# Kernel tuning notes

Hardware: AMD Instinct MI355X
Metric: run time of the kernel (lower is better)

Reference implementation:

```python
import jax, jax.numpy as jnp
import numpy as np

COL = 14
NJ = 14
SIGMA = 1.0
RADIUS = 4  # int(truncate*sigma + 0.5) with scipy defaults truncate=4.0
B = 8192
C = NJ + 4  # 14 joint channels + 4 group channels


def _gauss_kernel():
    x = np.arange(-RADIUS, RADIUS + 1).astype(np.float32)
    k = np.exp(-0.5 * x * x / (SIGMA * SIGMA))
    return jnp.asarray(k / k.sum(), jnp.float32)


def _gaussian_filter(x):
    # x: [N, H, W]; scipy gaussian_filter(sigma=1.0, mode='reflect') == symmetric pad + separable conv
    k = _gauss_kernel()
    xp = jnp.pad(x, ((0, 0), (RADIUS, RADIUS), (RADIUS, RADIUS)), mode='symmetric')
    y = jax.lax.conv_general_dilated(xp[:, None, :, :], k.reshape(1, 1, 2 * RADIUS + 1, 1), (1, 1), 'VALID')
    y = jax.lax.conv_general_dilated(y, k.reshape(1, 1, 1, 2 * RADIUS + 1), (1, 1), 'VALID')
    return y[:, 0]


def setup_inputs() -> dict:
    key = jax.random.key(0)
    k1, k2, k3, k4 = jax.random.split(key, 4)
    return {
        'os': jax.random.normal(k1, (B, 2 * NJ, COL, COL), dtype=jnp.float32),
        'h': jax.random.normal(k2, (B, C, COL, COL), dtype=jnp.float32),
        't': jax.random.uniform(k3, (B, NJ, 2), dtype=jnp.float32),
        'v': jax.random.randint(k4, (B, NJ, 2), 0, 2, dtype=jnp.int32),
    }


def reference(os, h, t, v):
    b = h.shape[0]
    # pixel indices: int() truncation then clamp to [0, 13]
    ti = jax.lax.stop_gradient(t) * COL
    idx = jnp.clip(ti.astype(jnp.int32), 0, COL - 1)
    xi, yi = idx[..., 0], idx[..., 1]
    vis = (v[..., 0] == 1)  # [B, NJ]

    ar = jnp.arange(COL)
    onehot = ((ar[:, None] == yi[..., None, None]) & (ar[None, :] == xi[..., None, None])).astype(h.dtype)  # [B,NJ,14,14]
    joint_hot = onehot * vis[..., None, None].astype(h.dtype)

    # 4 group channels from joints 0:3, 3:6, 6:9, 9:12 (set to 1, i.e. max, not add)
    ghot = joint_hot[:, :12].reshape(b, 4, 3, COL, COL).max(axis=2)
    gvis = vis[:, :12].reshape(b, 4, 3).any(axis=2)

    hot = jnp.concatenate([joint_hot, ghot], axis=1)        # [B, 18, 14, 14]
    mask = jnp.concatenate([vis, gvis], axis=1)             # [B, 18]

    filt = _gaussian_filter(hot.reshape(b * C, COL, COL)).reshape(b, C, COL, COL)
    mn = filt.min(axis=(-2, -1), keepdims=True)
    mx = filt.max(axis=(-2, -1), keepdims=True)
    denom = jnp.where(mx - mn == 0, jnp.ones_like(mx), mx - mn)
    tt = jnp.where(mask[..., None, None], (filt - mn) / denom, jnp.zeros_like(filt))

    diff = (h - tt) * mask[..., None, None].astype(h.dtype)
    n1 = v.sum().astype(h.dtype) / 2
    return jnp.sum(diff * diff) / n1
```

## Files before the change

### kernel.cpp

```cpp
#include <hip/hip_runtime.h>

#define NB   8192
#define NJ   14
#define NC   18
#define PIX  196
#define CHE  (NC * PIX)
#define CHB  (PIX * 4)
#define BPB  8
#define NBLK (NB / BPB)
#define GSTR 16
#define ZROW 14

#define WSUM_INV 0.398943491f

__global__ __launch_bounds__(512, 8) void mse_partial_kernel(
    const float* __restrict__ h, const float* __restrict__ t,
    const int* __restrict__ v, float2* __restrict__ partials)
{
    __shared__ float  gs[15 * GSTR];
    __shared__ float  gmx[14];
    __shared__ int    scode[BPB * 16];
    __shared__ float2 list[BPB * NC];
    __shared__ float  wvs[BPB];
    __shared__ float  wred[BPB];

    const int tid = threadIdx.x;
    const int b0  = blockIdx.x * BPB;
    const int w   = tid >> 6, lane = tid & 63;
    const int b   = b0 + w;

    if (tid < 15 * GSTR) {
        int p = tid >> 4, r = tid & 15;
        int rc = (r < 14) ? r : (r - 14);
        float val = 0.f;
        if (p < 14) {
            const float wl[9] = {0.00033546262f, 0.011108997f, 0.13533528f, 0.60653066f,
                                 1.0f, 0.60653066f, 0.13533528f, 0.011108997f, 0.00033546262f};
            float acc = 0.f;
            #pragma unroll
            for (int k = 0; k < 9; k++) {
                int m  = rc + k - 4;
                int sm = m < 0 ? (-m - 1) : (m > 13 ? 27 - m : m);
                if (sm == p) acc += wl[k];
            }
            val = acc * WSUM_INV;
        }
        gs[tid] = val;
    }
    __syncthreads();
    if (tid < 14) {
        float mx = 0.f;
        #pragma unroll
        for (int r = 0; r < 14; r++) mx = fmaxf(mx, gs[tid * GSTR + r]);
        gmx[tid] = mx;
    }
    __syncthreads();

    int rb_[4], cb_[4];
    #pragma unroll
    for (int q = 0; q < 4; q++) {
        int e = lane + 64 * q;
        int ee = (e < PIX) ? e : PIX - 1;
        int rr = ee / 14, cc = ee - 14 * rr;
        rb_[q] = rr << 2; cb_[q] = cc << 2;
    }

    int xi = 0, yi = 0, vis = 0, vy = 0;
    if (lane < NJ) {
        float2 tv = ((const float2*)t)[b * NJ + lane];
        int2   vv = ((const int2*)v)[b * NJ + lane];
        xi = (int)(tv.x * 14.0f); xi = xi < 0 ? 0 : (xi > 13 ? 13 : xi);
        yi = (int)(tv.y * 14.0f); yi = yi < 0 ? 0 : (yi > 13 ? 13 : yi);
        vis = (vv.x == 1); vy = (vv.y == 1);
    }
    if (lane < NJ) scode[w * 16 + lane] = (vis << 8) | (xi << 4) | yi;
    {
        unsigned long long bx = __ballot(lane < NJ && vis);
        unsigned long long by = __ballot(lane < NJ && vy);
        if (lane == 0) wvs[w] = (float)(__popcll(bx) + __popcll(by));
    }

    float inv_c = 0.f;
    int   pos_c = 0, act_c = 0, np_c = 0;
    if (lane < NJ && vis) {
        inv_c = 1.f / (gmx[yi] * gmx[xi]);
        act_c = 1; np_c = 1;
        pos_c = yi | (xi << 4) | (ZROW << 8) | (ZROW << 16);
    }
    for (int gi = 0; gi < 4; gi++) {
        int c0  = __builtin_amdgcn_readfirstlane(scode[w * 16 + 3 * gi]);
        int c1_ = __builtin_amdgcn_readfirstlane(scode[w * 16 + 3 * gi + 1]);
        int c2  = __builtin_amdgcn_readfirstlane(scode[w * 16 + 3 * gi + 2]);
        int packed = 0, np = 0;
        if (c0 & 0x100) { packed = c0 & 0xFF; np = 1; }
        if (c1_ & 0x100) {
            int pc = c1_ & 0xFF;
            bool dup = (np > 0) && ((packed & 0xFF) == pc);
            if (!dup) { packed |= pc << (8 * np); np++; }
        }
        if (c2 & 0x100) {
            int pc = c2 & 0xFF;
            bool dup = false;
            for (int s = 0; s < np; s++) if (((packed >> (8 * s)) & 0xFF) == pc) dup = true;
            if (!dup) { packed |= pc << (8 * np); np++; }
        }
        int pp = packed;
        if (np < 2) pp |= ZROW << 8;
        if (np < 3) pp |= ZROW << 16;

        float mx = 1.f;
        if (np == 1) {
            int y = packed & 15, x = (packed >> 4) & 15;
            mx = gmx[y] * gmx[x];
        } else if (np >= 2) {
            const int o0 = ( pp        & 15) << 6, p0 = ((pp >> 4)  & 15) << 6;
            const int o1 = ((pp >> 8)  & 15) << 6, p1 = ((pp >> 12) & 15) << 6;
            const int o2 = ((pp >> 16) & 15) << 6, p2 = ((pp >> 20) & 15) << 6;
            const char* g8 = (const char*)gs;
            float lmx = 0.f;
            #pragma unroll
            for (int q2 = 0; q2 < 4; q2++) {
                float f = *(const float*)(g8 + o0 + rb_[q2]) * *(const float*)(g8 + p0 + cb_[q2])
                        + *(const float*)(g8 + o1 + rb_[q2]) * *(const float*)(g8 + p1 + cb_[q2])
                        + *(const float*)(g8 + o2 + rb_[q2]) * *(const float*)(g8 + p2 + cb_[q2]);
                lmx = fmaxf(lmx, f);
            }
            #pragma unroll
            for (int m = 1; m < 64; m <<= 1)
                lmx = fmaxf(lmx, __shfl_xor(lmx, m));
            mx = lmx;
        }
        if (lane == NJ + gi && np > 0) {
            inv_c = 1.f / mx; act_c = 1; np_c = np;
            pos_c = pp;
        }
    }
    unsigned long long b1 = __ballot(act_c && np_c == 1);
    unsigned long long bX = __ballot(act_c && np_c >= 2);
    const int c1 = __popcll(b1);
    const int cT = c1 + __popcll(bX);
    unsigned long long below = (1ull << lane) - 1ull;
    if (act_c) {
        int idx = (np_c == 1) ? __popcll(b1 & below) : c1 + __popcll(bX & below);
        float2 e;
        e.x = inv_c;
        e.y = __int_as_float(pos_c | (lane << 24));
        list[w * NC + idx] = e;
    }

    const char* hb   = (const char*)(h + (size_t)b * CHE);
    const int  lane49 = lane < 48 ? lane : 48;
    const bool lv     = (lane < 49);
    const int  pix0   = lane49 * 4;
    const int  rr0    = pix0 / 14;
    const int  cc0    = pix0 - 14 * rr0;
    const bool wrap   = (cc0 == 12);
    const int  voff   = lane49 * 16;
    const int  brr = rr0 << 2, bcc = cc0 << 2;
    const int  lbase  = w * NC;
    const char* g8 = (const char*)gs;
    float acc = 0.f;

    const int nfull = c1 & ~3;
    for (int base = 0; base < nfull; base += 4) {
        float inv[4];
        int   syo[4], sxo[4], sb[4];
        float4 hv[4];
        #pragma unroll
        for (int u = 0; u < 4; u++) {
            float2 mv = list[lbase + base + u];
            inv[u] = mv.x;
            int sp = __builtin_amdgcn_readfirstlane(__float_as_int(mv.y));
            syo[u] = ( sp       & 15) << 6;
            sxo[u] = ((sp >> 4) & 15) << 6;
            sb[u]  = (sp >> 24) * CHB;
            hv[u] = *(const float4*)(hb + sb[u] + voff);
        }
        #pragma unroll
        for (int u = 0; u < 4; u++) {
            const float* ry = (const float*)(g8 + syo[u] + brr);
            const char*  rx = g8 + sxo[u] + bcc;
            float2 xA = *(const float2*)rx;
            float2 xB = *(const float2*)(rx + 8);
            float wy0 = ry[0], wy1 = ry[1];
            float wy0i = wy0 * inv[u];
            float wyCi = (wrap ? wy1 : wy0) * inv[u];
            float d0 = fmaf(-wy0i, xA.x, hv[u].x);
            float d1 = fmaf(-wy0i, xA.y, hv[u].y);
            float d2 = fmaf(-wyCi, xB.x, hv[u].z);
            float d3 = fmaf(-wyCi, xB.y, hv[u].w);
            acc += fmaf(d0, d0, fmaf(d1, d1, fmaf(d2, d2, d3 * d3)));
        }
    }
    if (c1 & 3) {
        float inv[4];
        int   syo[4], sxo[4], sb[4], ok[4];
        float4 hv[4];
        #pragma unroll
        for (int u = 0; u < 4; u++) {
            int ee = nfull + u;
            ok[u] = (ee < c1);
            float2 mv = list[lbase + (ok[u] ? ee : c1 - 1)];
            inv[u] = mv.x;
            int sp = __builtin_amdgcn_readfirstlane(__float_as_int(mv.y));
            syo[u] = ( sp       & 15) << 6;
            sxo[u] = ((sp >> 4) & 15) << 6;
            sb[u]  = (sp >> 24) * CHB;
            hv[u] = *(const float4*)(hb + sb[u] + voff);
        }
        #pragma unroll
        for (int u = 0; u < 4; u++) {
            const float* ry = (const float*)(g8 + syo[u] + brr);
            const char*  rx = g8 + sxo[u] + bcc;
            float2 xA = *(const float2*)rx;
            float2 xB = *(const float2*)(rx + 8);
            float wy0 = ry[0], wy1 = ry[1];
            float wy0i = wy0 * inv[u];
            float wyCi = (wrap ? wy1 : wy0) * inv[u];
            float d0 = fmaf(-wy0i, xA.x, hv[u].x);
            float d1 = fmaf(-wy0i, xA.y, hv[u].y);
            float d2 = fmaf(-wyCi, xB.x, hv[u].z);
            float d3 = fmaf(-wyCi, xB.y, hv[u].w);
            float s  = fmaf(d0, d0, fmaf(d1, d1, fmaf(d2, d2, d3 * d3)));
            acc += ok[u] ? s : 0.f;
        }
    }

    for (int e = c1; e < cT; e++) {
        float2 mv = list[lbase + e];
        float inv = mv.x;
        int sp = __builtin_amdgcn_readfirstlane(__float_as_int(mv.y));
        int sb = (sp >> 24) * CHB;
        float4 hv = *(const float4*)(hb + sb + voff);
        float f0 = 0.f, f1 = 0.f, f2 = 0.f, f3 = 0.f;
        #pragma unroll
        for (int q = 0; q < 3; q++) {
            int yo = ((sp >> (8 * q))     & 15) << 6;
            int xo = ((sp >> (8 * q + 4)) & 15) << 6;
            const float* ry = (const float*)(g8 + yo + brr);
            const char*  rx = g8 + xo + bcc;
            float2 xA = *(const float2*)rx;
            float2 xB = *(const float2*)(rx + 8);
            float wy0 = ry[0], wy1 = ry[1];
            float wyC = wrap ? wy1 : wy0;
            f0 = fmaf(wy0, xA.x, f0);
            f1 = fmaf(wy0, xA.y, f1);
            f2 = fmaf(wyC, xB.x, f2);
            f3 = fmaf(wyC, xB.y, f3);
        }
        float d0 = fmaf(-f0, inv, hv.x);
        float d1 = fmaf(-f1, inv, hv.y);
        float d2 = fmaf(-f2, inv, hv.z);
        float d3 = fmaf(-f3, inv, hv.w);
        acc += fmaf(d0, d0, fmaf(d1, d1, fmaf(d2, d2, d3 * d3)));
    }

    acc = lv ? acc : 0.f;

    #pragma unroll
    for (int off = 32; off > 0; off >>= 1) acc += __shfl_down(acc, off);
    if (lane == 0) wred[w] = acc;
    __syncthreads();
    if (tid == 0) {
        float2 pr;
        float s = 0.f, vs = 0.f;
        #pragma unroll
        for (int q = 0; q < BPB; q++) { s += wred[q]; vs += wvs[q]; }
        pr.x = s; pr.y = vs;
        partials[blockIdx.x] = pr;
    }
}

__global__ __launch_bounds__(512) void finalize_kernel(
    const float4* __restrict__ partials4, float* __restrict__ out)
{
    __shared__ float w1[8], w2[8];
    int tid = threadIdx.x;
    float4 p = partials4[tid];
    float s = p.x + p.z, vs = p.y + p.w;
    #pragma unroll
    for (int off = 32; off > 0; off >>= 1) {
        s  += __shfl_down(s, off);
        vs += __shfl_down(vs, off);
    }
    if ((tid & 63) == 0) { w1[tid >> 6] = s; w2[tid >> 6] = vs; }
    __syncthreads();
    if (tid == 0) {
        float stot = 0.f, vtot = 0.f;
        #pragma unroll
        for (int q = 0; q < 8; q++) { stot += w1[q]; vtot += w2[q]; }
        out[0] = stot / (vtot * 0.5f);
    }
}

extern "C" void kernel_launch(void* const* d_in, const int* in_sizes, int n_in,
                              void* d_out, int out_size, void* d_ws, size_t ws_size,
                              hipStream_t stream) {
    const float* h = (const float*)d_in[1];
    const float* t = (const float*)d_in[2];
    const int*   v = (const int*)d_in[3];
    float2* partials = (float2*)d_ws;

    mse_partial_kernel<<<NBLK, 512, 0, stream>>>(h, t, v, partials);
    finalize_kernel<<<1, 512, 0, stream>>>((const float4*)partials, (float*)d_out);
}
```

Measured before the change: 21.54 us.

## Double-buffer heatmap loads across chunks and lower occupancy hint

Replaces the chunked loop over visible channels with a fully unrolled, double-buffered schedule. The next chunk's global h loads are issued before the current chunk is computed, so memory latency overlaps with arithmetic. The launch-bounds minimum of waves per EU drops from 8 to 6, giving the compiler more registers for the two in-flight chunks at the cost of occupancy. The hard-coded schedule covers at most five chunks (20 entries), which matches the 18 channels.

```diff
diff --git a/kernel.cpp b/kernel.cpp
--- a/kernel.cpp
+++ b/kernel.cpp
@@ -13,7 +13,13 @@
 
 #define WSUM_INV 0.398943491f
 
-__global__ __launch_bounds__(512, 8) void mse_partial_kernel(
+struct Chunk {
+    float4 hv[4];
+    float  inv[4];
+    int    syo[4], sxo[4];
+};
+
+__global__ __launch_bounds__(512, 6) void mse_partial_kernel(
     const float* __restrict__ h, const float* __restrict__ t,
     const int* __restrict__ v, float2* __restrict__ partials)
 {
@@ -161,70 +167,52 @@
     const char* g8 = (const char*)gs;
     float acc = 0.f;
 
-    const int nfull = c1 & ~3;
-    for (int base = 0; base < nfull; base += 4) {
-        float inv[4];
-        int   syo[4], sxo[4], sb[4];
-        float4 hv[4];
+    Chunk cA, cB;
+
+    auto STAGE = [&](Chunk& C, int base4) {
         #pragma unroll
         for (int u = 0; u < 4; u++) {
-            float2 mv = list[lbase + base + u];
-            inv[u] = mv.x;
+            int ee = base4 + u;
+            ee = (ee < c1) ? ee : c1 - 1;
+            float2 mv = list[lbase + ee];
+            C.inv[u] = mv.x;
             int sp = __builtin_amdgcn_readfirstlane(__float_as_int(mv.y));
-            syo[u] = ( sp       & 15) << 6;
-            sxo[u] = ((sp >> 4) & 15) << 6;
-            sb[u]  = (sp >> 24) * CHB;
-            hv[u] = *(const float4*)(hb + sb[u] + voff);
-        }
+            C.syo[u] = ( sp       & 15) << 6;
+            C.sxo[u] = ((sp >> 4) & 15) << 6;
+            int sb = (sp >> 24) * CHB;
+            C.hv[u] = *(const float4*)(hb + sb + voff);
+        }
+    };
+    auto COMP = [&](Chunk& C, int base4) {
         #pragma unroll
         for (int u = 0; u < 4; u++) {
-            const float* ry = (const float*)(g8 + syo[u] + brr);
-            const char*  rx = g8 + sxo[u] + bcc;
+            const float* ry = (const float*)(g8 + C.syo[u] + brr);
+            const char*  rx = g8 + C.sxo[u] + bcc;
             float2 xA = *(const float2*)rx;
             float2 xB = *(const float2*)(rx + 8);
             float wy0 = ry[0], wy1 = ry[1];
-            float wy0i = wy0 * inv[u];
-            float wyCi = (wrap ? wy1 : wy0) * inv[u];
-            float d0 = fmaf(-wy0i, xA.x, hv[u].x);
-            float d1 = fmaf(-wy0i, xA.y, hv[u].y);
-            float d2 = fmaf(-wyCi, xB.x, hv[u].z);
-            float d3 = fmaf(-wyCi, xB.y, hv[u].w);
-            acc += fmaf(d0, d0, fmaf(d1, d1, fmaf(d2, d2, d3 * d3)));
-        }
-    }
-    if (c1 & 3) {
-        float inv[4];
-        int   syo[4], sxo[4], sb[4], ok[4];
-        float4 hv[4];
-        #pragma unroll
-        for (int u = 0; u < 4; u++) {
-            int ee = nfull + u;
-            ok[u] = (ee < c1);
-            float2 mv = list[lbase + (ok[u] ? ee : c1 - 1)];
-            inv[u] = mv.x;
-            int sp = __builtin_amdgcn_readfirstlane(__float_as_int(mv.y));
-            syo[u] = ( sp       & 15) << 6;
-            sxo[u] = ((sp >> 4) & 15) << 6;
-            sb[u]  = (sp >> 24) * CHB;
-            hv[u] = *(const float4*)(hb + sb[u] + voff);
-        }
-        #pragma unroll
-        for (int u = 0; u < 4; u++) {
-            const float* ry = (const float*)(g8 + syo[u] + brr);
-            const char*  rx = g8 + sxo[u] + bcc;
-            float2 xA = *(const float2*)rx;
-            float2 xB = *(const float2*)(rx + 8);
-            float wy0 = ry[0], wy1 = ry[1];
-            float wy0i = wy0 * inv[u];
-            float wyCi = (wrap ? wy1 : wy0) * inv[u];
-            float d0 = fmaf(-wy0i, xA.x, hv[u].x);
-            float d1 = fmaf(-wy0i, xA.y, hv[u].y);
-            float d2 = fmaf(-wyCi, xB.x, hv[u].z);
-            float d3 = fmaf(-wyCi, xB.y, hv[u].w);
+            float wy0i = wy0 * C.inv[u];
+            float wyCi = (wrap ? wy1 : wy0) * C.inv[u];
+            float d0 = fmaf(-wy0i, xA.x, C.hv[u].x);
+            float d1 = fmaf(-wy0i, xA.y, C.hv[u].y);
+            float d2 = fmaf(-wyCi, xB.x, C.hv[u].z);
+            float d3 = fmaf(-wyCi, xB.y, C.hv[u].w);
             float s  = fmaf(d0, d0, fmaf(d1, d1, fmaf(d2, d2, d3 * d3)));
-            acc += ok[u] ? s : 0.f;
-        }
-    }
+            acc += (base4 + u < c1) ? s : 0.f;
+        }
+    };
+
+    const int nch = (c1 + 3) >> 2;
+    if (nch > 0) STAGE(cA, 0);
+    if (nch > 1) STAGE(cB, 4);
+    if (nch > 0) COMP (cA, 0);
+    if (nch > 2) STAGE(cA, 8);
+    if (nch > 1) COMP (cB, 4);
+    if (nch > 3) STAGE(cB, 12);
+    if (nch > 2) COMP (cA, 8);
+    if (nch > 4) STAGE(cA, 16);
+    if (nch > 3) COMP (cB, 12);
+    if (nch > 4) COMP (cA, 16);
 
     for (int e = c1; e < cT; e++) {
         float2 mv = list[lbase + e];
```

Result: slower. 27.40 us (+27.2%).
